# Performance work log

Hardware: AMD Instinct MI355X
Metric: run time of the kernel (lower is better)

Reference implementation:

```python
import jax, jax.numpy as jnp
import numpy as np

DIM = 192
HEADS = 6
WIN = (2, 6, 12)          # (pl, lat, lon)
TOW = 64                  # type_of_windows = (8//2)*(96//6)
N_TOK = WIN[0] * WIN[1] * WIN[2]            # 144
TABLE_ROWS = WIN[0]**2 * WIN[1]**2 * (2 * WIN[2] - 1)  # 3312


def calc_position_bias_indices(size):
    pl, la, lo = size
    plq = np.arange(pl); plk = -np.arange(pl) * pl
    laq = np.arange(la); lak = -np.arange(la) * la
    lon = np.arange(lo)
    gq = np.stack(np.meshgrid(plq, laq, lon, indexing='ij'))  # [3,pl,la,lo]
    gk = np.stack(np.meshgrid(plk, lak, lon, indexing='ij'))
    fq = gq.reshape(3, -1)
    fk = gk.reshape(3, -1)
    d = fq[:, :, None] - fk[:, None, :]          # [3,N,N]
    d = np.transpose(d, (1, 2, 0)).copy()
    d[:, :, 2] += lo - 1
    d[:, :, 1] *= 2 * lo - 1
    d[:, :, 0] *= (2 * lo - 1) * la * la
    return d.sum(-1)                              # [N,N]


def setup_inputs() -> dict:
    key = jax.random.key(0)
    ks = jax.random.split(key, 7)
    B_, nW, N, C = 15, TOW, N_TOK, DIM
    x = jax.random.normal(ks[0], (B_, nW, N, C), jnp.float32)
    mask = jax.random.normal(ks[1], (15, nW, N, N), jnp.float32)  # nLon=15
    qkv_w = jax.random.normal(ks[2], (3 * C, C), jnp.float32) * 0.02
    qkv_b = jnp.zeros((3 * C,), jnp.float32)
    table = jax.random.normal(ks[3], (TABLE_ROWS, TOW, HEADS), jnp.float32) * 0.02
    proj_w = jax.random.normal(ks[4], (C, C), jnp.float32) * 0.02
    proj_b = jnp.zeros((C,), jnp.float32)
    pos_index = jnp.asarray(calc_position_bias_indices(WIN), jnp.int32)  # [N,N]
    return {"x": x, "mask": mask, "qkv_w": qkv_w, "qkv_b": qkv_b,
            "table": table, "proj_w": proj_w, "proj_b": proj_b,
            "pos_index": pos_index}


def reference(x, mask, qkv_w, qkv_b, table, proj_w, proj_b, pos_index):
    B_, nW, N, C = x.shape
    h = HEADS
    hd = C // h
    scale = hd ** -0.5
    # qkv projection -> (3, B_, h, nW, N, hd)
    qkv = (jnp.einsum('bwnc,dc->bwnd', x, qkv_w) + qkv_b)
    qkv = qkv.reshape(B_, nW, N, 3, h, hd).transpose(3, 0, 4, 1, 2, 5)
    q, k, v = qkv[0] * scale, qkv[1], qkv[2]
    attn = jnp.einsum('bhwqd,bhwkd->bhwqk', q, k)      # [B_,h,nW,N,N]
    # gather earth position bias: [N,N,tow,h] -> [h,tow,N,N]
    bias = table[pos_index.reshape(-1)].reshape(N, N, nW, h)
    bias = bias.transpose(3, 2, 0, 1)
    attn = attn + bias[None]
    nLon = mask.shape[0]
    attn = attn.reshape(B_ // nLon, nLon, h, nW, N, N) + mask[None, :, None]
    attn = attn.reshape(B_, h, nW, N, N)
    attn = jax.nn.softmax(attn, axis=-1)
    out = jnp.einsum('bhwqk,bhwkd->bhwqd', attn, v)
    out = out.transpose(0, 2, 3, 1, 4).reshape(B_, nW, N, C)
    return jnp.einsum('bwnc,dc->bwnd', out, proj_w) + proj_b
```

## Files before the change

kernel.cpp:

```cpp
#include <hip/hip_runtime.h>

#define HEADS 6
#define N_TOK 144
#define DIM   192
#define NW    64
#define NB    15
#define NBW   (NB * NW)
#define CHUNK 480

typedef __attribute__((ext_vector_type(8))) short bf16x8;
typedef __attribute__((ext_vector_type(4))) float f32x4;

#define MFMA(a, b, c) __builtin_amdgcn_mfma_f32_16x16x32_bf16(a, b, c, 0, 0, 0)

static __device__ __forceinline__ short f2bf(float f) {
    union { float f; unsigned u; } v; v.f = f;
    unsigned r = v.u + 0x7FFFu + ((v.u >> 16) & 1u);
    return (short)(r >> 16);
}
static __device__ __forceinline__ float bf2f(short s) {
    union { unsigned u; float f; } v;
    v.u = ((unsigned)(unsigned short)s) << 16;
    return v.f;
}
static __device__ __forceinline__ unsigned pk2(float a, float b) {
    return (unsigned)(unsigned short)f2bf(a) |
           ((unsigned)(unsigned short)f2bf(b) << 16);
}

__global__ __launch_bounds__(256)
void bias_k(const float* __restrict__ table, const int* __restrict__ pos_index,
            short* __restrict__ bias_bf) {
    const int t = blockIdx.x;
    for (int e = threadIdx.x; e < N_TOK * N_TOK; e += 256) {
        int idx = pos_index[e];
        bias_bf[(long)t * (N_TOK * N_TOK) + e] = f2bf(table[(long)idx * 384 + t]);
    }
}

__global__ __launch_bounds__(256)
void cvt_k(const float* __restrict__ w, short* __restrict__ o, int n) {
    int i = blockIdx.x * 256 + threadIdx.x;
    if (i < n) o[i] = f2bf(w[i]);
}

__global__ __launch_bounds__(256)
void cvtx_k(const float* __restrict__ x, short* __restrict__ xb, int n4) {
    int i = blockIdx.x * 256 + threadIdx.x;
    if (i < n4) {
        float4 f = ((const float4*)x)[i];
        short4 s = { f2bf(f.x), f2bf(f.y), f2bf(f.z), f2bf(f.w) };
        ((short4*)xb)[i] = s;
    }
}

__global__ __launch_bounds__(576)
void qkvs_k(const short* __restrict__ xb, const short* __restrict__ qkvw_bf,
            const float* __restrict__ qkv_b, short* __restrict__ qk_ws,
            short* __restrict__ vT_ws) {
    __shared__ short wlds[192 * 200];

    const int sel = blockIdx.x % 3;
    const int bwL = blockIdx.x / 3;
    const int tid = threadIdx.x;

    for (int u = tid * 8; u < 192 * 192; u += 576 * 8) {
        int r = u / 192, c = u - r * 192;
        *(bf16x8*)&wlds[r * 200 + c] = *(const bf16x8*)&qkvw_bf[sel * 36864 + u];
    }
    __syncthreads();

    const int wid = tid >> 6, lane = tid & 63, lq = lane & 15, lg = lane >> 4;
    const int mg = wid / 3, ng = wid % 3;
    const short* xrow = xb + (long)bwL * N_TOK * DIM;

    f32x4 acc[3][4] = {};
    for (int ks = 0; ks < 6; ++ks) {
        const int k0 = ks * 32 + 8 * lg;
        bf16x8 av[3], bv[4];
        #pragma unroll
        for (int mt = 0; mt < 3; ++mt)
            av[mt] = *(const bf16x8*)&xrow[(mg * 48 + mt * 16 + lq) * DIM + k0];
        #pragma unroll
        for (int nt = 0; nt < 4; ++nt)
            bv[nt] = *(const bf16x8*)&wlds[(ng * 64 + nt * 16 + lq) * 200 + k0];
        #pragma unroll
        for (int mt = 0; mt < 3; ++mt)
            #pragma unroll
            for (int nt = 0; nt < 4; ++nt)
                acc[mt][nt] = MFMA(av[mt], bv[nt], acc[mt][nt]);
    }
    __syncthreads();

    const float scale = 0.17677669529663687f;

    if (sel < 2) {
        #pragma unroll
        for (int nt = 0; nt < 4; ++nt) {
            const int cd = ng * 64 + nt * 16 + lq;
            const float bb = qkv_b[sel * 192 + cd];
            #pragma unroll
            for (int mt = 0; mt < 3; ++mt)
                #pragma unroll
                for (int i = 0; i < 4; ++i) {
                    int row = mg * 48 + mt * 16 + 4 * lg + i;
                    float v = acc[mt][nt][i] + bb;
                    if (sel == 0) v *= scale;
                    wlds[row * 200 + cd] = f2bf(v);
                }
        }
        __syncthreads();
        short* ob = qk_ws + (long)bwL * 6 * 2 * 4608 + (long)sel * 4608;
        #pragma unroll
        for (int j = 0; j < 6; ++j) {
            int u = (j * 576 + tid) * 8;
            int h = u / 4608, rem = u - h * 4608;
            *(bf16x8*)&ob[(long)h * 2 * 4608 + rem] =
                *(const bf16x8*)&wlds[(rem >> 5) * 200 + h * 32 + (rem & 31)];
        }
    } else {
        #pragma unroll
        for (int nt = 0; nt < 4; ++nt) {
            const int cd = ng * 64 + nt * 16 + lq;
            const float bb = qkv_b[2 * 192 + cd];
            #pragma unroll
            for (int mt = 0; mt < 3; ++mt)
                #pragma unroll
                for (int i = 0; i < 4; ++i) {
                    int row = mg * 48 + mt * 16 + 4 * lg + i;
                    wlds[cd * 152 + row] = f2bf(acc[mt][nt][i] + bb);
                }
        }
        __syncthreads();
        short* ob = vT_ws + (long)bwL * 6 * 4608;
        #pragma unroll
        for (int j = 0; j < 6; ++j) {
            int u = (j * 576 + tid) * 8;
            int h = u / 4608, rem = u - h * 4608;
            int e = rem / 144, row0 = rem - e * 144;
            *(bf16x8*)&ob[(long)h * 4608 + e * 144 + row0] =
                *(const bf16x8*)&wlds[(h * 32 + e) * 152 + row0];
        }
    }
}

__global__ __launch_bounds__(192, 6)
void attn3w_k(const short* __restrict__ qk_ws, const short* __restrict__ vT_ws,
              const short* __restrict__ bias_bf, const float* __restrict__ mask,
              short* __restrict__ tmp, int bw0) {
    __shared__ short pws[3 * 16 * 168];

    const int p = blockIdx.x;
    const int l = (p & 7) * 1080 + (p >> 3);
    const int third = l % 3;
    const int h     = (l / 3) % HEADS;
    const int bwL   = l / 18;
    const int bwG   = bw0 + bwL;
    const int lane = threadIdx.x & 63, lq = lane & 15, lg = lane >> 4;
    const int wid = threadIdx.x >> 6;
    const int mt9 = third * 3 + wid;
    const int q = mt9 * 16 + lq;
    const int w = bwG & 63;

    const short* qb = qk_ws + (long)(bwL * 6 + h) * 2 * 4608;
    const short* kb = qb + 4608;

    const f32x4 zf = {};
    bf16x8 bq = *(const bf16x8*)&qb[q * 32 + 8 * lg];
    f32x4 lgt[9];
    #pragma unroll
    for (int nt = 0; nt < 9; ++nt) {
        bf16x8 ak = *(const bf16x8*)&kb[(nt * 16 + lq) * 32 + 8 * lg];
        lgt[nt] = MFMA(ak, bq, zf);
    }

    const short* bp = bias_bf + (long)(w * 6 + h) * (N_TOK * N_TOK)
                    + q * N_TOK + 4 * lg;
    const float* mp = mask + (long)bwG * (N_TOK * N_TOK) + q * N_TOK + 4 * lg;
    #pragma unroll
    for (int nt = 0; nt < 9; ++nt) {
        short4 bs = *(const short4*)&bp[nt * 16];
        float4 mf = *(const float4*)&mp[nt * 16];
        lgt[nt][0] += bf2f(bs.x) + mf.x;
        lgt[nt][1] += bf2f(bs.y) + mf.y;
        lgt[nt][2] += bf2f(bs.z) + mf.z;
        lgt[nt][3] += bf2f(bs.w) + mf.w;
    }

    float m = lgt[0][0];
    #pragma unroll
    for (int nt = 0; nt < 9; ++nt)
        #pragma unroll
        for (int i = 0; i < 4; ++i) m = fmaxf(m, lgt[nt][i]);
    m = fmaxf(m, __shfl_xor(m, 16));
    m = fmaxf(m, __shfl_xor(m, 32));
    float s = 0.f;
    #pragma unroll
    for (int nt = 0; nt < 9; ++nt)
        #pragma unroll
        for (int i = 0; i < 4; ++i) {
            float pe = __expf(lgt[nt][i] - m);
            lgt[nt][i] = pe;
            s += pe;
        }
    s += __shfl_xor(s, 16);
    s += __shfl_xor(s, 32);
    const float inv = 1.f / s;

    short* pw = pws + wid * 16 * 168;
    #pragma unroll
    for (int nt = 0; nt < 9; ++nt) {
        *(unsigned*)&pw[lq * 168 + nt * 16 + 4 * lg]     = pk2(lgt[nt][0], lgt[nt][1]);
        *(unsigned*)&pw[lq * 168 + nt * 16 + 4 * lg + 2] = pk2(lgt[nt][2], lgt[nt][3]);
    }

    const short* vsrc = vT_ws + (long)(bwL * 6 + h) * 4608;
    f32x4 o[2] = {};
    const bf16x8 zb = {};
    #pragma unroll
    for (int kt = 0; kt < 5; ++kt) {
        bf16x8 bpf = *(const bf16x8*)&pw[lq * 168 + kt * 32 + 8 * lg];
        #pragma unroll
        for (int et = 0; et < 2; ++et) {
            bf16x8 av = *(const bf16x8*)&vsrc[(et * 16 + lq) * N_TOK + kt * 32 + 8 * lg];
            bf16x8 aa = av, bb = bpf;
            if (kt == 4 && lg >= 2) { aa = zb; bb = zb; }
            o[et] = MFMA(aa, bb, o[et]);
        }
    }

    short* tb = tmp + ((long)bwL * N_TOK + q) * DIM + h * 32;
    #pragma unroll
    for (int et = 0; et < 2; ++et) {
        short4 sx = { f2bf(o[et][0] * inv), f2bf(o[et][1] * inv),
                      f2bf(o[et][2] * inv), f2bf(o[et][3] * inv) };
        *(short4*)&tb[et * 16 + 4 * lg] = sx;
    }
}

__global__ __launch_bounds__(192)
void proj_k(const short* __restrict__ tmp, const short* __restrict__ pwt,
            const float* __restrict__ proj_b, float* __restrict__ out, int bw0) {
    const int bid = blockIdx.x;
    const int mthird = bid % 3;
    const int bwL = bid / 3;
    const int bwG = bw0 + bwL;
    const int tid = threadIdx.x;
    const int wid = tid >> 6, lane = tid & 63, lq = lane & 15, lg = lane >> 4;
    const int m0 = (mthird * 3 + wid) * 16;
    const short* tb = tmp + (long)bwL * N_TOK * DIM;

    f32x4 acc[12] = {};
    for (int ks = 0; ks < 6; ++ks) {
        const int k0 = ks * 32 + 8 * lg;
        bf16x8 a = *(const bf16x8*)&tb[(m0 + lq) * DIM + k0];
        #pragma unroll
        for (int nt = 0; nt < 12; ++nt) {
            bf16x8 b = *(const bf16x8*)&pwt[(nt * 16 + lq) * DIM + k0];
            acc[nt] = MFMA(a, b, acc[nt]);
        }
    }
    float* ob = out + (long)bwG * N_TOK * DIM;
    #pragma unroll
    for (int nt = 0; nt < 12; ++nt) {
        float pb = proj_b[nt * 16 + lq];
        #pragma unroll
        for (int i = 0; i < 4; ++i)
            ob[(m0 + 4 * lg + i) * DIM + nt * 16 + lq] = acc[nt][i] + pb;
    }
}

extern "C" void kernel_launch(void* const* d_in, const int* in_sizes, int n_in,
                              void* d_out, int out_size, void* d_ws, size_t ws_size,
                              hipStream_t stream) {
    const float* x        = (const float*)d_in[0];
    const float* mask     = (const float*)d_in[1];
    const float* qkv_w    = (const float*)d_in[2];
    const float* qkv_b    = (const float*)d_in[3];
    const float* table    = (const float*)d_in[4];
    const float* proj_w   = (const float*)d_in[5];
    const float* proj_b   = (const float*)d_in[6];
    const int*   pos_index= (const int*)d_in[7];
    float* out = (float*)d_out;

    short* bias_bf  = (short*)d_ws;
    short* projw_bf = bias_bf + (size_t)384 * N_TOK * N_TOK;
    short* qkvw_bf  = projw_bf + 36864;
    short* xbf_ws   = qkvw_bf + 110592;
    short* tmp_ws   = xbf_ws;
    short* qk_ws    = xbf_ws + (size_t)CHUNK * N_TOK * DIM;
    short* vT_ws    = qk_ws + (size_t)CHUNK * 6 * 2 * 4608;

    bias_k<<<384, 256, 0, stream>>>(table, pos_index, bias_bf);
    cvt_k<<<144, 256, 0, stream>>>(proj_w, projw_bf, DIM * DIM);
    cvt_k<<<432, 256, 0, stream>>>(qkv_w, qkvw_bf, 3 * DIM * DIM);

    const int n4 = CHUNK * N_TOK * DIM / 4;
    for (int c = 0; c < 2; ++c) {
        const int bw0 = c * CHUNK;
        cvtx_k<<<(n4 + 255) / 256, 256, 0, stream>>>(
            x + (long)bw0 * N_TOK * DIM, xbf_ws, n4);
        qkvs_k<<<CHUNK * 3, 576, 0, stream>>>(xbf_ws, qkvw_bf, qkv_b,
                                              qk_ws, vT_ws);
        attn3w_k<<<CHUNK * 18, 192, 0, stream>>>(qk_ws, vT_ws, bias_bf, mask,
                                                 tmp_ws, bw0);
        proj_k<<<CHUNK * 3, 192, 0, stream>>>(tmp_ws, projw_bf, proj_b, out, bw0);
    }
}
```

Before: 446.8 us.

## Fuse x bf16 conversion into QKV kernel and split blocks by row group

Removes the separate fp32-to-bf16 conversion kernel for x and its round trip through workspace, converting x tiles directly into LDS inside the QKV projection kernel. The QKV kernel is restructured from 576-thread blocks covering all 144 rows to 192-thread blocks each handling a 48-row group for one of q/k/v, with weights now read from global or L2 rather than staged in LDS. This cuts launches and global traffic and lowers LDS use per block, at the cost of repeated weight fetches from global memory by every block.

```diff
diff --git a/kernel.cpp b/kernel.cpp
--- a/kernel.cpp
+++ b/kernel.cpp
@@ -44,35 +44,33 @@
     if (i < n) o[i] = f2bf(w[i]);
 }
 
-__global__ __launch_bounds__(256)
-void cvtx_k(const float* __restrict__ x, short* __restrict__ xb, int n4) {
-    int i = blockIdx.x * 256 + threadIdx.x;
-    if (i < n4) {
-        float4 f = ((const float4*)x)[i];
-        short4 s = { f2bf(f.x), f2bf(f.y), f2bf(f.z), f2bf(f.w) };
-        ((short4*)xb)[i] = s;
-    }
-}
-
-__global__ __launch_bounds__(576)
-void qkvs_k(const short* __restrict__ xb, const short* __restrict__ qkvw_bf,
-            const float* __restrict__ qkv_b, short* __restrict__ qk_ws,
-            short* __restrict__ vT_ws) {
-    __shared__ short wlds[192 * 200];
-
-    const int sel = blockIdx.x % 3;
-    const int bwL = blockIdx.x / 3;
+__global__ __launch_bounds__(192)
+void qkvs192_k(const float* __restrict__ x, const short* __restrict__ qkvw_bf,
+               const float* __restrict__ qkv_b, short* __restrict__ qk_ws,
+               short* __restrict__ vT_ws, int bw0) {
+    __shared__ short xl[192 * 56];
+
+    const int p = blockIdx.x;
+    const int l = (p & 7) * 540 + (p >> 3);
+    const int mg  = l % 3;
+    const int sel = (l / 3) % 3;
+    const int bwL = l / 9;
+    const int bwG = bw0 + bwL;
     const int tid = threadIdx.x;
 
-    for (int u = tid * 8; u < 192 * 192; u += 576 * 8) {
-        int r = u / 192, c = u - r * 192;
-        *(bf16x8*)&wlds[r * 200 + c] = *(const bf16x8*)&qkvw_bf[sel * 36864 + u];
+    {
+        const float* xg = x + ((long)bwG * N_TOK + mg * 48) * DIM;
+        for (int u = tid * 4; u < 48 * DIM; u += 192 * 4) {
+            float4 f = *(const float4*)&xg[u];
+            short4 s = { f2bf(f.x), f2bf(f.y), f2bf(f.z), f2bf(f.w) };
+            int r = u / DIM, c = u - r * DIM;
+            *(short4*)&xl[r * 200 + c] = s;
+        }
     }
     __syncthreads();
 
     const int wid = tid >> 6, lane = tid & 63, lq = lane & 15, lg = lane >> 4;
-    const int mg = wid / 3, ng = wid % 3;
-    const short* xrow = xb + (long)bwL * N_TOK * DIM;
+    const int ng = wid;
 
     f32x4 acc[3][4] = {};
     for (int ks = 0; ks < 6; ++ks) {
@@ -80,10 +78,11 @@
         bf16x8 av[3], bv[4];
         #pragma unroll
         for (int mt = 0; mt < 3; ++mt)
-            av[mt] = *(const bf16x8*)&xrow[(mg * 48 + mt * 16 + lq) * DIM + k0];
+            av[mt] = *(const bf16x8*)&xl[(mt * 16 + lq) * 200 + k0];
         #pragma unroll
         for (int nt = 0; nt < 4; ++nt)
-            bv[nt] = *(const bf16x8*)&wlds[(ng * 64 + nt * 16 + lq) * 200 + k0];
+            bv[nt] = *(const bf16x8*)&qkvw_bf[
+                ((long)sel * 192 + ng * 64 + nt * 16 + lq) * 192 + k0];
         #pragma unroll
         for (int mt = 0; mt < 3; ++mt)
             #pragma unroll
@@ -103,20 +102,22 @@
             for (int mt = 0; mt < 3; ++mt)
                 #pragma unroll
                 for (int i = 0; i < 4; ++i) {
-                    int row = mg * 48 + mt * 16 + 4 * lg + i;
+                    int row = mt * 16 + 4 * lg + i;
                     float v = acc[mt][nt][i] + bb;
                     if (sel == 0) v *= scale;
-                    wlds[row * 200 + cd] = f2bf(v);
+                    xl[row * 200 + cd] = f2bf(v);
                 }
         }
         __syncthreads();
-        short* ob = qk_ws + (long)bwL * 6 * 2 * 4608 + (long)sel * 4608;
+        short* ob = qk_ws + (long)bwL * 6 * 2 * 4608 + (long)sel * 4608
+                  + mg * 48 * 32;
         #pragma unroll
         for (int j = 0; j < 6; ++j) {
-            int u = (j * 576 + tid) * 8;
-            int h = u / 4608, rem = u - h * 4608;
-            *(bf16x8*)&ob[(long)h * 2 * 4608 + rem] =
-                *(const bf16x8*)&wlds[(rem >> 5) * 200 + h * 32 + (rem & 31)];
+            int u = (j * 192 + tid) * 8;
+            int h = u / 1536, rem = u - h * 1536;
+            int row = rem >> 5, e = rem & 31;
+            *(bf16x8*)&ob[(long)h * 2 * 4608 + row * 32 + e] =
+                *(const bf16x8*)&xl[row * 200 + h * 32 + e];
         }
     } else {
         #pragma unroll
@@ -127,19 +128,18 @@
             for (int mt = 0; mt < 3; ++mt)
                 #pragma unroll
                 for (int i = 0; i < 4; ++i) {
-                    int row = mg * 48 + mt * 16 + 4 * lg + i;
-                    wlds[cd * 152 + row] = f2bf(acc[mt][nt][i] + bb);
+                    int row = mt * 16 + 4 * lg + i;
+                    xl[cd * 56 + row] = f2bf(acc[mt][nt][i] + bb);
                 }
         }
         __syncthreads();
-        short* ob = vT_ws + (long)bwL * 6 * 4608;
+        short* ob = vT_ws + (long)bwL * 6 * 4608 + mg * 48;
         #pragma unroll
         for (int j = 0; j < 6; ++j) {
-            int u = (j * 576 + tid) * 8;
-            int h = u / 4608, rem = u - h * 4608;
-            int e = rem / 144, row0 = rem - e * 144;
-            *(bf16x8*)&ob[(long)h * 4608 + e * 144 + row0] =
-                *(const bf16x8*)&wlds[(h * 32 + e) * 152 + row0];
+            int u = (j * 192 + tid) * 8;
+            int he = u / 48, row0 = u - he * 48;
+            *(bf16x8*)&ob[(long)he * 144 + row0] =
+                *(const bf16x8*)&xl[he * 56 + row0];
         }
     }
 }
@@ -286,22 +286,18 @@
     short* bias_bf  = (short*)d_ws;
     short* projw_bf = bias_bf + (size_t)384 * N_TOK * N_TOK;
     short* qkvw_bf  = projw_bf + 36864;
-    short* xbf_ws   = qkvw_bf + 110592;
-    short* tmp_ws   = xbf_ws;
-    short* qk_ws    = xbf_ws + (size_t)CHUNK * N_TOK * DIM;
+    short* tmp_ws   = qkvw_bf + 110592;
+    short* qk_ws    = tmp_ws + (size_t)CHUNK * N_TOK * DIM;
     short* vT_ws    = qk_ws + (size_t)CHUNK * 6 * 2 * 4608;
 
     bias_k<<<384, 256, 0, stream>>>(table, pos_index, bias_bf);
     cvt_k<<<144, 256, 0, stream>>>(proj_w, projw_bf, DIM * DIM);
     cvt_k<<<432, 256, 0, stream>>>(qkv_w, qkvw_bf, 3 * DIM * DIM);
 
-    const int n4 = CHUNK * N_TOK * DIM / 4;
     for (int c = 0; c < 2; ++c) {
         const int bw0 = c * CHUNK;
-        cvtx_k<<<(n4 + 255) / 256, 256, 0, stream>>>(
-            x + (long)bw0 * N_TOK * DIM, xbf_ws, n4);
-        qkvs_k<<<CHUNK * 3, 576, 0, stream>>>(xbf_ws, qkvw_bf, qkv_b,
-                                              qk_ws, vT_ws);
+        qkvs192_k<<<CHUNK * 9, 192, 0, stream>>>(x, qkvw_bf, qkv_b,
+                                                 qk_ws, vT_ws, bw0);
         attn3w_k<<<CHUNK * 18, 192, 0, stream>>>(qk_ws, vT_ws, bias_bf, mask,
                                                  tmp_ws, bw0);
         proj_k<<<CHUNK * 3, 192, 0, stream>>>(tmp_ws, projw_bf, proj_b, out, bw0);
```

After: 464.5 us. 1.04x slower.
